# Kernel optimization log

Measured on AMD Instinct MI355X. Metric: run time of the kernel, lower is better.

Reference implementation:

```python
import math
import jax, jax.numpy as jnp
import numpy as np

B, H, HKV, L, S, D = 1, 32, 8, 2048, 2048, 128
N_REP = H // HKV          # 4
SCALE = 1.0 / math.sqrt(D)


def setup_inputs() -> dict:
    key = jax.random.key(0)
    k1, k2, k3, k4 = jax.random.split(key, 4)
    query = jax.random.normal(k1, (B, H, L, D), dtype=jnp.float32)
    k_ = jax.random.normal(k2, (B, HKV, S, D), dtype=jnp.float32)
    v_ = jax.random.normal(k3, (B, HKV, S, D), dtype=jnp.float32)
    attn_mask = jax.random.normal(k4, (B, 1, L, S), dtype=jnp.float32)
    return {"query": query, "key": k_, "value": v_, "attn_mask": attn_mask}


def reference(query, key, value, attn_mask):
    # repeat_kv: Q -> [B, HKV, n_rep, L, D]; K/V stay [B, HKV, S, D]
    # (the torch code reshapes K/V to [B, HKV, 1, S, D]; broadcasting via
    # einsum is equivalent), mask unsqueezed at dim 1 -> [B, 1, 1, L, S].
    q = query.reshape(B, HKV, N_REP, L, D)
    scores = jnp.einsum("bkrld,bksd->bkrls", q, key)          # [B,HKV,n_rep,L,S]
    scores = scores + attn_mask[:, None]                        # broadcast add
    # softmax_fp8(x, dim=-1, invAttnHead=1/sqrt(D)) scales input by invAttnHead
    w = jax.nn.softmax(scores * SCALE, axis=-1)
    # dropout_p = 0.0 -> identity
    out = jnp.einsum("bkrls,bksd->bkrld", w, value)             # [B,HKV,n_rep,L,D]
    return out
```

## Files before the change

kernel.cpp:

```cpp
#include <hip/hip_runtime.h>

#define NH   32
#define NKV  8
#define LQ   2048
#define SK   2048
#define DH   128
#define BM   128
#define BN   64
#define NT   (SK / BN)
#define VSTRIDE 72

typedef __attribute__((ext_vector_type(8)))  short bf8;
typedef __attribute__((ext_vector_type(16))) float f16v;
typedef __attribute__((ext_vector_type(4)))  unsigned int u32x4;

#define CL2E 0.12754308753f

#if __has_builtin(__builtin_amdgcn_exp2f)
#define EXP2F(x) __builtin_amdgcn_exp2f(x)
#else
#define EXP2F(x) exp2f(x)
#endif

__device__ __forceinline__ unsigned short f2bf(float f) {
    unsigned int u = __builtin_bit_cast(unsigned int, f);
    u = (u + 0x7FFFu + ((u >> 16) & 1u)) >> 16;
    return (unsigned short)u;
}

__device__ __forceinline__ unsigned int cvtpk_bf16(float lo, float hi) {
    unsigned int r;
    asm("v_cvt_pk_bf16_f32 %0, %1, %2" : "=v"(r) : "v"(lo), "v"(hi));
    return r;
}

__device__ __forceinline__ float bflo(unsigned int u) {
    return __builtin_bit_cast(float, u << 16);
}
__device__ __forceinline__ float bfhi(unsigned int u) {
    return __builtin_bit_cast(float, u & 0xFFFF0000u);
}

#define GLOAD_LDS16(g, l)                                                      \
    __builtin_amdgcn_global_load_lds(                                          \
        (const __attribute__((address_space(1))) void*)(g),                    \
        (__attribute__((address_space(3))) void*)(l), 16, 0, 0)

__global__ __launch_bounds__(256) void convert_k_kernel(
    const float* __restrict__ K, unsigned short* __restrict__ Kb)
{
    unsigned int cid = blockIdx.x * 256 + threadIdx.x;
    unsigned int p   = cid & 15;
    unsigned int row = cid >> 4;
    unsigned int s   = row & (SK - 1);
    unsigned int c   = p ^ (s & 15);
    const float* src = K + (size_t)row * DH + c * 8;
    float4 a = *(const float4*)(src);
    float4 b = *(const float4*)(src + 4);
    bf8 o;
    o[0] = (short)f2bf(a.x); o[1] = (short)f2bf(a.y);
    o[2] = (short)f2bf(a.z); o[3] = (short)f2bf(a.w);
    o[4] = (short)f2bf(b.x); o[5] = (short)f2bf(b.y);
    o[6] = (short)f2bf(b.z); o[7] = (short)f2bf(b.w);
    *(bf8*)(Kb + (size_t)row * DH + p * 8) = o;
}

__global__ __launch_bounds__(256) void transpose_v_kernel(
    const float* __restrict__ V, unsigned short* __restrict__ VTb)
{
    __shared__ __align__(16) unsigned short Vl[DH * VSTRIDE];
    const int tid = threadIdx.x;
    const int kv  = blockIdx.x >> 5;
    const int t   = blockIdx.x & 31;
    const int s0  = t * 64;
    const float* Vh = V + (size_t)kv * SK * DH;

    #pragma unroll
    for (int i = 0; i < 8; ++i) {
        int idx = tid * 4 + i * 1024;
        int s = idx >> 7, d = idx & 127;
        const float4 v4 = *(const float4*)(Vh + (size_t)(s0 + s) * DH + d);
        Vl[(d + 0) * VSTRIDE + s] = f2bf(v4.x);
        Vl[(d + 1) * VSTRIDE + s] = f2bf(v4.y);
        Vl[(d + 2) * VSTRIDE + s] = f2bf(v4.z);
        Vl[(d + 3) * VSTRIDE + s] = f2bf(v4.w);
    }
    __syncthreads();
    unsigned short* out = VTb + (size_t)(kv * 32 + t) * (DH * 64);
    #pragma unroll
    for (int i = 0; i < 4; ++i) {
        int c = tid + i * 256;
        int d = c >> 3, p = c & 7;
        int sc = (p ^ (d & 7)) * 8;
        *(bf8*)(out + d * 64 + p * 8) = *(const bf8*)(Vl + d * VSTRIDE + sc);
    }
}

__global__ __launch_bounds__(256) void convert_m_kernel(
    const float* __restrict__ M, unsigned short* __restrict__ Mb)
{
    unsigned int cid = blockIdx.x * 256 + threadIdx.x;
    unsigned int row = cid >> 8;
    unsigned int l   = (cid & 255) * 8;
    unsigned int T   = l & ~63u;
    unsigned int loc = l & 63;
    unsigned int mt = loc >> 5, w = loc & 31;
    unsigned int hh = w >> 4, g0 = (w >> 2) & 3;
    const float* src = M + (size_t)row * SK + T + mt * 32 + hh * 4;
    float4 a = *(const float4*)(src + g0 * 8);
    float4 b = *(const float4*)(src + (g0 + 1) * 8);
    bf8 o;
    o[0] = (short)f2bf(a.x * CL2E); o[1] = (short)f2bf(a.y * CL2E);
    o[2] = (short)f2bf(a.z * CL2E); o[3] = (short)f2bf(a.w * CL2E);
    o[4] = (short)f2bf(b.x * CL2E); o[5] = (short)f2bf(b.y * CL2E);
    o[6] = (short)f2bf(b.z * CL2E); o[7] = (short)f2bf(b.w * CL2E);
    *(bf8*)(Mb + (size_t)row * SK + l) = o;
}

__global__ __launch_bounds__(256, 2) void fattn_kernel(
    const float* __restrict__ Q, const unsigned short* __restrict__ Kb,
    const unsigned short* __restrict__ VTb, const unsigned short* __restrict__ Mb,
    float* __restrict__ O)
{
    __shared__ __align__(1024) unsigned char smem[65536];
    unsigned char* KB = smem;
    unsigned char* VB = smem + 32768;

    const int tid  = threadIdx.x;
    const int wave = tid >> 6;
    const int lane = tid & 63;
    const int l32  = lane & 31;
    const int hh   = lane >> 5;

    const int bx = ((int)blockIdx.x & 7) * 64 + ((int)blockIdx.x >> 3);
    const int h  = bx >> 4;
    const int lt = bx & 15;
    const int q0 = lt * BM;
    const int kv = h >> 2;

    const float* Qh = Q + (size_t)h * LQ * DH;
    const unsigned char* Kg = (const unsigned char*)(Kb  + (size_t)kv * SK * DH);
    const unsigned char* Vg = (const unsigned char*)(VTb + (size_t)kv * SK * DH);

    const int qrow = q0 + wave * 32 + l32;
    const unsigned short* Mq = Mb + (size_t)qrow * SK + hh * 16;

    bf8 bQ[8];
    {
        const float* qp = Qh + (size_t)qrow * DH + hh * 8;
        #pragma unroll
        for (int ks = 0; ks < 8; ++ks) {
            float4 a = *(const float4*)(qp + ks * 16);
            float4 b = *(const float4*)(qp + ks * 16 + 4);
            bf8 o;
            o[0] = (short)f2bf(a.x); o[1] = (short)f2bf(a.y);
            o[2] = (short)f2bf(a.z); o[3] = (short)f2bf(a.w);
            o[4] = (short)f2bf(b.x); o[5] = (short)f2bf(b.y);
            o[6] = (short)f2bf(b.z); o[7] = (short)f2bf(b.w);
            bQ[ks] = o;
        }
    }

    const int krow0 = l32 * 256 + ((hh * 16) ^ ((l32 & 15) << 4));
    const int vrowz = l32 * 128 + ((hh * 16) ^ ((l32 & 7) << 4));

    const int stoff = wave * 4096 + lane * 16;

    f16v accO[4];
    #pragma unroll
    for (int dt = 0; dt < 4; ++dt)
        #pragma unroll
        for (int r = 0; r < 16; ++r) accO[dt][r] = 0.f;
    float lpart = 0.f;

    #pragma unroll
    for (int c = 0; c < 4; ++c) GLOAD_LDS16(Kg + stoff + c * 1024, KB + stoff + c * 1024);
    #pragma unroll
    for (int c = 0; c < 4; ++c) GLOAD_LDS16(Vg + stoff + c * 1024, VB + stoff + c * 1024);

    for (int t = 0; t < NT; ++t) {
        const int cur = t & 1;

        const unsigned short* mp = Mq + t * 64;
        u32x4 mA0 = *(const u32x4*)(mp);
        u32x4 mB0 = *(const u32x4*)(mp + 8);
        u32x4 mA1 = *(const u32x4*)(mp + 32);
        u32x4 mB1 = *(const u32x4*)(mp + 40);
        __builtin_amdgcn_sched_barrier(0);

        {
            const int tn = (t + 1) & (NT - 1);
            const unsigned char* ksrc = Kg + (size_t)tn * 16384 + stoff;
            const unsigned char* vsrc = Vg + (size_t)tn * 16384 + stoff;
            unsigned char* kdst = KB + (cur ^ 1) * 16384 + stoff;
            unsigned char* vdst = VB + (cur ^ 1) * 16384 + stoff;
            #pragma unroll
            for (int c = 0; c < 4; ++c) GLOAD_LDS16(ksrc + c * 1024, kdst + c * 1024);
            #pragma unroll
            for (int c = 0; c < 4; ++c) GLOAD_LDS16(vsrc + c * 1024, vdst + c * 1024);
        }
        __builtin_amdgcn_sched_barrier(0);
        asm volatile("s_waitcnt vmcnt(12)" ::: "memory");
        __builtin_amdgcn_s_barrier();
        asm volatile("" ::: "memory");

        const unsigned char* kb = KB + cur * 16384;
        const unsigned char* vb = VB + cur * 16384;

        unsigned int pk0[8], pk1[8];
        #pragma unroll
        for (int mt = 0; mt < 2; ++mt) {
            f16v s;
            #pragma unroll
            for (int r = 0; r < 16; ++r) s[r] = 0.f;
            __builtin_amdgcn_s_setprio(1);
            #pragma unroll
            for (int ks = 0; ks < 8; ++ks) {
                bf8 aK = *(const bf8*)(kb + mt * 8192 + (krow0 ^ (ks << 5)));
                s = __builtin_amdgcn_mfma_f32_32x32x16_bf16(aK, bQ[ks], s, 0, 0, 0);
            }
            __builtin_amdgcn_s_setprio(0);
            const u32x4 mA = mt ? mA1 : mA0;
            const u32x4 mB = mt ? mB1 : mB0;
            unsigned int* pk = mt ? pk1 : pk0;
            #pragma unroll
            for (int g = 0; g < 4; ++g) {
                unsigned int u0 = (g < 2) ? mA[g * 2 + 0] : mB[(g - 2) * 2 + 0];
                unsigned int u1 = (g < 2) ? mA[g * 2 + 1] : mB[(g - 2) * 2 + 1];
                float e0 = EXP2F(fmaf(s[g*4+0], CL2E, bflo(u0)));
                float e1 = EXP2F(fmaf(s[g*4+1], CL2E, bfhi(u0)));
                float e2 = EXP2F(fmaf(s[g*4+2], CL2E, bflo(u1)));
                float e3 = EXP2F(fmaf(s[g*4+3], CL2E, bfhi(u1)));
                lpart += (e0 + e1) + (e2 + e3);
                pk[g*2+0] = cvtpk_bf16(e0, e1);
                pk[g*2+1] = cvtpk_bf16(e2, e3);
            }
        }

        bf8 bP[4];
        #pragma unroll
        for (int ks = 0; ks < 4; ++ks) {
            unsigned int* pk = (ks >> 1) ? pk1 : pk0;
            const int kk = ks & 1;
            unsigned int a0 = pk[kk*4+0], b0 = pk[kk*4+2];
            unsigned int a1 = pk[kk*4+1], b1 = pk[kk*4+3];
            asm volatile("v_permlane32_swap_b32 %0, %1" : "+v"(a0), "+v"(b0));
            asm volatile("v_permlane32_swap_b32 %0, %1" : "+v"(a1), "+v"(b1));
            u32x4 w; w[0] = a0; w[1] = a1; w[2] = b0; w[3] = b1;
            bP[ks] = __builtin_bit_cast(bf8, w);
        }

        __builtin_amdgcn_s_setprio(1);
        #pragma unroll
        for (int dt = 0; dt < 4; ++dt) {
            #pragma unroll
            for (int ks = 0; ks < 4; ++ks) {
                bf8 aV = *(const bf8*)(vb + dt * 4096 + (vrowz ^ (ks << 5)));
                accO[dt] = __builtin_amdgcn_mfma_f32_32x32x16_bf16(aV, bP[ks], accO[dt], 0, 0, 0);
            }
        }
        __builtin_amdgcn_s_setprio(0);
        asm volatile("" ::: "memory");
        __builtin_amdgcn_s_barrier();
        asm volatile("" ::: "memory");
    }

    asm volatile("s_waitcnt vmcnt(0)" ::: "memory");
    float l = lpart + __shfl_xor(lpart, 32);
    float inv = 1.0f / l;
    float* Op = O + (size_t)h * LQ * DH + (size_t)qrow * DH;
    #pragma unroll
    for (int dt = 0; dt < 4; ++dt) {
        #pragma unroll
        for (int g = 0; g < 4; ++g) {
            int d = dt * 32 + g * 8 + hh * 4;
            float4 o;
            o.x = accO[dt][g * 4 + 0] * inv;
            o.y = accO[dt][g * 4 + 1] * inv;
            o.z = accO[dt][g * 4 + 2] * inv;
            o.w = accO[dt][g * 4 + 3] * inv;
            *(float4*)(Op + d) = o;
        }
    }
}

extern "C" void kernel_launch(void* const* d_in, const int* in_sizes, int n_in,
                              void* d_out, int out_size, void* d_ws, size_t ws_size,
                              hipStream_t stream) {
    const float* Q = (const float*)d_in[0];
    const float* K = (const float*)d_in[1];
    const float* V = (const float*)d_in[2];
    const float* M = (const float*)d_in[3];
    float* O = (float*)d_out;

    unsigned short* Kb  = (unsigned short*)d_ws;
    unsigned short* VTb = Kb + (size_t)NKV * SK * DH;
    unsigned short* Mb  = VTb + (size_t)NKV * DH * SK;

    convert_k_kernel<<<dim3((NKV * SK * 16) / 256), 256, 0, stream>>>(K, Kb);
    transpose_v_kernel<<<dim3(NKV * (SK / 64)), 256, 0, stream>>>(V, VTb);
    convert_m_kernel<<<dim3((LQ * (SK / 8)) / 256), 256, 0, stream>>>(M, Mb);

    dim3 grid(NH * (LQ / BM));
    fattn_kernel<<<grid, 256, 0, stream>>>(Q, Kb, VTb, Mb, O);
}
```

Measured before the change: 185.1 us.

## Split KV tile across wave pairs, halve query tile, merge prep kernels

Halves the query tile per block to 64 rows and splits each 64-key tile between pairs of waves, each handling 32 keys. Partial outputs and row sums are reduced through shared memory at the end. V is now staged through registers into a single LDS buffer, which cuts LDS to 48KB so three blocks fit per CU. The three preprocessing kernels are also merged into one launch. The aim is higher occupancy and fewer launches, at the cost of an extra cross-wave reduction and more grid blocks reloading K/V.

Result: slower. 228.0 us (+23.2%).

```diff
diff --git a/kernel.cpp b/kernel.cpp
--- a/kernel.cpp
+++ b/kernel.cpp
@@ -5,7 +5,7 @@
 #define LQ   2048
 #define SK   2048
 #define DH   128
-#define BM   128
+#define BM   64
 #define BN   64
 #define NT   (SK / BN)
 #define VSTRIDE 72
@@ -46,83 +46,81 @@
         (const __attribute__((address_space(1))) void*)(g),                    \
         (__attribute__((address_space(3))) void*)(l), 16, 0, 0)
 
-__global__ __launch_bounds__(256) void convert_k_kernel(
-    const float* __restrict__ K, unsigned short* __restrict__ Kb)
-{
-    unsigned int cid = blockIdx.x * 256 + threadIdx.x;
-    unsigned int p   = cid & 15;
-    unsigned int row = cid >> 4;
-    unsigned int s   = row & (SK - 1);
-    unsigned int c   = p ^ (s & 15);
-    const float* src = K + (size_t)row * DH + c * 8;
-    float4 a = *(const float4*)(src);
-    float4 b = *(const float4*)(src + 4);
-    bf8 o;
-    o[0] = (short)f2bf(a.x); o[1] = (short)f2bf(a.y);
-    o[2] = (short)f2bf(a.z); o[3] = (short)f2bf(a.w);
-    o[4] = (short)f2bf(b.x); o[5] = (short)f2bf(b.y);
-    o[6] = (short)f2bf(b.z); o[7] = (short)f2bf(b.w);
-    *(bf8*)(Kb + (size_t)row * DH + p * 8) = o;
-}
-
-__global__ __launch_bounds__(256) void transpose_v_kernel(
-    const float* __restrict__ V, unsigned short* __restrict__ VTb)
+__global__ __launch_bounds__(256) void prep_kernel(
+    const float* __restrict__ K, unsigned short* __restrict__ Kb,
+    const float* __restrict__ V, unsigned short* __restrict__ VTb,
+    const float* __restrict__ M, unsigned short* __restrict__ Mb)
 {
     __shared__ __align__(16) unsigned short Vl[DH * VSTRIDE];
     const int tid = threadIdx.x;
-    const int kv  = blockIdx.x >> 5;
-    const int t   = blockIdx.x & 31;
-    const int s0  = t * 64;
-    const float* Vh = V + (size_t)kv * SK * DH;
-
-    #pragma unroll
-    for (int i = 0; i < 8; ++i) {
-        int idx = tid * 4 + i * 1024;
-        int s = idx >> 7, d = idx & 127;
-        const float4 v4 = *(const float4*)(Vh + (size_t)(s0 + s) * DH + d);
-        Vl[(d + 0) * VSTRIDE + s] = f2bf(v4.x);
-        Vl[(d + 1) * VSTRIDE + s] = f2bf(v4.y);
-        Vl[(d + 2) * VSTRIDE + s] = f2bf(v4.z);
-        Vl[(d + 3) * VSTRIDE + s] = f2bf(v4.w);
-    }
-    __syncthreads();
-    unsigned short* out = VTb + (size_t)(kv * 32 + t) * (DH * 64);
-    #pragma unroll
-    for (int i = 0; i < 4; ++i) {
-        int c = tid + i * 256;
-        int d = c >> 3, p = c & 7;
-        int sc = (p ^ (d & 7)) * 8;
-        *(bf8*)(out + d * 64 + p * 8) = *(const bf8*)(Vl + d * VSTRIDE + sc);
-    }
-}
-
-__global__ __launch_bounds__(256) void convert_m_kernel(
-    const float* __restrict__ M, unsigned short* __restrict__ Mb)
-{
-    unsigned int cid = blockIdx.x * 256 + threadIdx.x;
-    unsigned int row = cid >> 8;
-    unsigned int l   = (cid & 255) * 8;
-    unsigned int T   = l & ~63u;
-    unsigned int loc = l & 63;
-    unsigned int mt = loc >> 5, w = loc & 31;
-    unsigned int hh = w >> 4, g0 = (w >> 2) & 3;
-    const float* src = M + (size_t)row * SK + T + mt * 32 + hh * 4;
-    float4 a = *(const float4*)(src + g0 * 8);
-    float4 b = *(const float4*)(src + (g0 + 1) * 8);
-    bf8 o;
-    o[0] = (short)f2bf(a.x * CL2E); o[1] = (short)f2bf(a.y * CL2E);
-    o[2] = (short)f2bf(a.z * CL2E); o[3] = (short)f2bf(a.w * CL2E);
-    o[4] = (short)f2bf(b.x * CL2E); o[5] = (short)f2bf(b.y * CL2E);
-    o[6] = (short)f2bf(b.z * CL2E); o[7] = (short)f2bf(b.w * CL2E);
-    *(bf8*)(Mb + (size_t)row * SK + l) = o;
-}
-
-__global__ __launch_bounds__(256, 2) void fattn_kernel(
+    const int bid = blockIdx.x;
+
+    if (bid < 1024) {
+        unsigned int cid = bid * 256 + tid;
+        unsigned int p   = cid & 15;
+        unsigned int row = cid >> 4;
+        unsigned int s   = row & (SK - 1);
+        unsigned int c   = p ^ (s & 15);
+        const float* src = K + (size_t)row * DH + c * 8;
+        float4 a = *(const float4*)(src);
+        float4 b = *(const float4*)(src + 4);
+        bf8 o;
+        o[0] = (short)f2bf(a.x); o[1] = (short)f2bf(a.y);
+        o[2] = (short)f2bf(a.z); o[3] = (short)f2bf(a.w);
+        o[4] = (short)f2bf(b.x); o[5] = (short)f2bf(b.y);
+        o[6] = (short)f2bf(b.z); o[7] = (short)f2bf(b.w);
+        *(bf8*)(Kb + (size_t)row * DH + p * 8) = o;
+    } else if (bid < 1280) {
+        const int vb = bid - 1024;
+        const int kv = vb >> 5;
+        const int t  = vb & 31;
+        const int s0 = t * 64;
+        const float* Vh = V + (size_t)kv * SK * DH;
+        #pragma unroll
+        for (int i = 0; i < 8; ++i) {
+            int idx = tid * 4 + i * 1024;
+            int s = idx >> 7, d = idx & 127;
+            const float4 v4 = *(const float4*)(Vh + (size_t)(s0 + s) * DH + d);
+            Vl[(d + 0) * VSTRIDE + s] = f2bf(v4.x);
+            Vl[(d + 1) * VSTRIDE + s] = f2bf(v4.y);
+            Vl[(d + 2) * VSTRIDE + s] = f2bf(v4.z);
+            Vl[(d + 3) * VSTRIDE + s] = f2bf(v4.w);
+        }
+        __syncthreads();
+        unsigned short* out = VTb + (size_t)(kv * 32 + t) * (DH * 64);
+        #pragma unroll
+        for (int i = 0; i < 4; ++i) {
+            int c = tid + i * 256;
+            int d = c >> 3, p = c & 7;
+            int sc = (p ^ (d & 7)) * 8;
+            *(bf8*)(out + d * 64 + p * 8) = *(const bf8*)(Vl + d * VSTRIDE + sc);
+        }
+    } else {
+        unsigned int cid = (bid - 1280) * 256 + tid;
+        unsigned int row = cid >> 8;
+        unsigned int l   = (cid & 255) * 8;
+        unsigned int T   = l & ~63u;
+        unsigned int loc = l & 63;
+        unsigned int mt = loc >> 5, w = loc & 31;
+        unsigned int hh = w >> 4, g0 = (w >> 2) & 3;
+        const float* src = M + (size_t)row * SK + T + mt * 32 + hh * 4;
+        float4 a = *(const float4*)(src + g0 * 8);
+        float4 b = *(const float4*)(src + (g0 + 1) * 8);
+        bf8 o;
+        o[0] = (short)f2bf(a.x * CL2E); o[1] = (short)f2bf(a.y * CL2E);
+        o[2] = (short)f2bf(a.z * CL2E); o[3] = (short)f2bf(a.w * CL2E);
+        o[4] = (short)f2bf(b.x * CL2E); o[5] = (short)f2bf(b.y * CL2E);
+        o[6] = (short)f2bf(b.z * CL2E); o[7] = (short)f2bf(b.w * CL2E);
+        *(bf8*)(Mb + (size_t)row * SK + l) = o;
+    }
+}
+
+__global__ __launch_bounds__(256, 3) void fattn_kernel(
     const float* __restrict__ Q, const unsigned short* __restrict__ Kb,
     const unsigned short* __restrict__ VTb, const unsigned short* __restrict__ Mb,
     float* __restrict__ O)
 {
-    __shared__ __align__(1024) unsigned char smem[65536];
+    __shared__ __align__(1024) unsigned char smem[49152];
     unsigned char* KB = smem;
     unsigned char* VB = smem + 32768;
 
@@ -131,10 +129,12 @@
     const int lane = tid & 63;
     const int l32  = lane & 31;
     const int hh   = lane >> 5;
-
-    const int bx = ((int)blockIdx.x & 7) * 64 + ((int)blockIdx.x >> 3);
-    const int h  = bx >> 4;
-    const int lt = bx & 15;
+    const int qg   = wave >> 1;
+    const int sg   = wave & 1;
+
+    const int bx = ((int)blockIdx.x & 7) * 128 + ((int)blockIdx.x >> 3);
+    const int h  = bx >> 5;
+    const int lt = bx & 31;
     const int q0 = lt * BM;
     const int kv = h >> 2;
 
@@ -142,8 +142,8 @@
     const unsigned char* Kg = (const unsigned char*)(Kb  + (size_t)kv * SK * DH);
     const unsigned char* Vg = (const unsigned char*)(VTb + (size_t)kv * SK * DH);
 
-    const int qrow = q0 + wave * 32 + l32;
-    const unsigned short* Mq = Mb + (size_t)qrow * SK + hh * 16;
+    const int qrow = q0 + qg * 32 + l32;
+    const unsigned short* Mq = Mb + (size_t)qrow * SK + sg * 32 + hh * 16;
 
     bf8 bQ[8];
     {
@@ -161,10 +161,8 @@
         }
     }
 
-    const int krow0 = l32 * 256 + ((hh * 16) ^ ((l32 & 15) << 4));
-    const int vrowz = l32 * 128 + ((hh * 16) ^ ((l32 & 7) << 4));
-
-    const int stoff = wave * 4096 + lane * 16;
+    const int krow0 = (sg * 32 + l32) * 256 + ((hh * 16) ^ ((l32 & 15) << 4));
+    const int vrow0 = l32 * 128 + ((sg * 64 + hh * 16) ^ ((l32 & 7) << 4));
 
     f16v accO[4];
     #pragma unroll
@@ -173,77 +171,78 @@
         for (int r = 0; r < 16; ++r) accO[dt][r] = 0.f;
     float lpart = 0.f;
 
-    #pragma unroll
-    for (int c = 0; c < 4; ++c) GLOAD_LDS16(Kg + stoff + c * 1024, KB + stoff + c * 1024);
-    #pragma unroll
-    for (int c = 0; c < 4; ++c) GLOAD_LDS16(Vg + stoff + c * 1024, VB + stoff + c * 1024);
+    {
+        const int so = wave * 1024 + lane * 16;
+        #pragma unroll
+        for (int c = 0; c < 4; ++c) GLOAD_LDS16(Kg + so + c * 4096, KB + so + c * 4096);
+        #pragma unroll
+        for (int c = 0; c < 4; ++c) GLOAD_LDS16(Vg + so + c * 4096, VB + so + c * 4096);
+    }
+
+    u32x4 vr0, vr1, vr2, vr3;
 
     for (int t = 0; t < NT; ++t) {
         const int cur = t & 1;
 
         const unsigned short* mp = Mq + t * 64;
-        u32x4 mA0 = *(const u32x4*)(mp);
-        u32x4 mB0 = *(const u32x4*)(mp + 8);
-        u32x4 mA1 = *(const u32x4*)(mp + 32);
-        u32x4 mB1 = *(const u32x4*)(mp + 40);
+        u32x4 mA = *(const u32x4*)(mp);
+        u32x4 mB = *(const u32x4*)(mp + 8);
         __builtin_amdgcn_sched_barrier(0);
 
+        const int tn = (t + 1) & (NT - 1);
         {
-            const int tn = (t + 1) & (NT - 1);
-            const unsigned char* ksrc = Kg + (size_t)tn * 16384 + stoff;
-            const unsigned char* vsrc = Vg + (size_t)tn * 16384 + stoff;
-            unsigned char* kdst = KB + (cur ^ 1) * 16384 + stoff;
-            unsigned char* vdst = VB + (cur ^ 1) * 16384 + stoff;
-            #pragma unroll
-            for (int c = 0; c < 4; ++c) GLOAD_LDS16(ksrc + c * 1024, kdst + c * 1024);
-            #pragma unroll
-            for (int c = 0; c < 4; ++c) GLOAD_LDS16(vsrc + c * 1024, vdst + c * 1024);
+            const unsigned char* vsrc = Vg + (size_t)tn * 16384 + tid * 64;
+            vr0 = *(const u32x4*)(vsrc);
+            vr1 = *(const u32x4*)(vsrc + 16);
+            vr2 = *(const u32x4*)(vsrc + 32);
+            vr3 = *(const u32x4*)(vsrc + 48);
         }
         __builtin_amdgcn_sched_barrier(0);
-        asm volatile("s_waitcnt vmcnt(12)" ::: "memory");
+
+        {
+            const unsigned char* ksrc = Kg + (size_t)tn * 16384;
+            unsigned char* kdst = KB + (cur ^ 1) * 16384;
+            const int so = wave * 1024 + lane * 16;
+            #pragma unroll
+            for (int c = 0; c < 4; ++c) GLOAD_LDS16(ksrc + so + c * 4096, kdst + so + c * 4096);
+        }
+        __builtin_amdgcn_sched_barrier(0);
+        asm volatile("s_waitcnt vmcnt(10) lgkmcnt(0)" ::: "memory");
         __builtin_amdgcn_s_barrier();
         asm volatile("" ::: "memory");
 
         const unsigned char* kb = KB + cur * 16384;
-        const unsigned char* vb = VB + cur * 16384;
-
-        unsigned int pk0[8], pk1[8];
-        #pragma unroll
-        for (int mt = 0; mt < 2; ++mt) {
-            f16v s;
-            #pragma unroll
-            for (int r = 0; r < 16; ++r) s[r] = 0.f;
-            __builtin_amdgcn_s_setprio(1);
-            #pragma unroll
-            for (int ks = 0; ks < 8; ++ks) {
-                bf8 aK = *(const bf8*)(kb + mt * 8192 + (krow0 ^ (ks << 5)));
-                s = __builtin_amdgcn_mfma_f32_32x32x16_bf16(aK, bQ[ks], s, 0, 0, 0);
-            }
-            __builtin_amdgcn_s_setprio(0);
-            const u32x4 mA = mt ? mA1 : mA0;
-            const u32x4 mB = mt ? mB1 : mB0;
-            unsigned int* pk = mt ? pk1 : pk0;
-            #pragma unroll
-            for (int g = 0; g < 4; ++g) {
-                unsigned int u0 = (g < 2) ? mA[g * 2 + 0] : mB[(g - 2) * 2 + 0];
-                unsigned int u1 = (g < 2) ? mA[g * 2 + 1] : mB[(g - 2) * 2 + 1];
-                float e0 = EXP2F(fmaf(s[g*4+0], CL2E, bflo(u0)));
-                float e1 = EXP2F(fmaf(s[g*4+1], CL2E, bfhi(u0)));
-                float e2 = EXP2F(fmaf(s[g*4+2], CL2E, bflo(u1)));
-                float e3 = EXP2F(fmaf(s[g*4+3], CL2E, bfhi(u1)));
-                lpart += (e0 + e1) + (e2 + e3);
-                pk[g*2+0] = cvtpk_bf16(e0, e1);
-                pk[g*2+1] = cvtpk_bf16(e2, e3);
-            }
-        }
-
-        bf8 bP[4];
-        #pragma unroll
-        for (int ks = 0; ks < 4; ++ks) {
-            unsigned int* pk = (ks >> 1) ? pk1 : pk0;
-            const int kk = ks & 1;
-            unsigned int a0 = pk[kk*4+0], b0 = pk[kk*4+2];
-            unsigned int a1 = pk[kk*4+1], b1 = pk[kk*4+3];
+
+        f16v s;
+        #pragma unroll
+        for (int r = 0; r < 16; ++r) s[r] = 0.f;
+        __builtin_amdgcn_s_setprio(1);
+        #pragma unroll
+        for (int ks = 0; ks < 8; ++ks) {
+            bf8 aK = *(const bf8*)(kb + (krow0 ^ (ks << 5)));
+            s = __builtin_amdgcn_mfma_f32_32x32x16_bf16(aK, bQ[ks], s, 0, 0, 0);
+        }
+        __builtin_amdgcn_s_setprio(0);
+
+        unsigned int pk[8];
+        #pragma unroll
+        for (int g = 0; g < 4; ++g) {
+            unsigned int u0 = (g < 2) ? mA[g * 2 + 0] : mB[(g - 2) * 2 + 0];
+            unsigned int u1 = (g < 2) ? mA[g * 2 + 1] : mB[(g - 2) * 2 + 1];
+            float e0 = EXP2F(fmaf(s[g*4+0], CL2E, bflo(u0)));
+            float e1 = EXP2F(fmaf(s[g*4+1], CL2E, bfhi(u0)));
+            float e2 = EXP2F(fmaf(s[g*4+2], CL2E, bflo(u1)));
+            float e3 = EXP2F(fmaf(s[g*4+3], CL2E, bfhi(u1)));
+            lpart += (e0 + e1) + (e2 + e3);
+            pk[g*2+0] = cvtpk_bf16(e0, e1);
+            pk[g*2+1] = cvtpk_bf16(e2, e3);
+        }
+
+        bf8 bP[2];
+        #pragma unroll
+        for (int ks = 0; ks < 2; ++ks) {
+            unsigned int a0 = pk[ks*4+0], b0 = pk[ks*4+2];
+            unsigned int a1 = pk[ks*4+1], b1 = pk[ks*4+3];
             asm volatile("v_permlane32_swap_b32 %0, %1" : "+v"(a0), "+v"(b0));
             asm volatile("v_permlane32_swap_b32 %0, %1" : "+v"(a1), "+v"(b1));
             u32x4 w; w[0] = a0; w[1] = a1; w[2] = b0; w[3] = b1;
@@ -254,8 +253,8 @@
         #pragma unroll
         for (int dt = 0; dt < 4; ++dt) {
             #pragma unroll
-            for (int ks = 0; ks < 4; ++ks) {
-                bf8 aV = *(const bf8*)(vb + dt * 4096 + (vrowz ^ (ks << 5)));
+            for (int ks = 0; ks < 2; ++ks) {
+                bf8 aV = *(const bf8*)(VB + dt * 4096 + (vrow0 ^ (ks << 5)));
                 accO[dt] = __builtin_amdgcn_mfma_f32_32x32x16_bf16(aV, bP[ks], accO[dt], 0, 0, 0);
             }
         }
@@ -263,23 +262,73 @@
         asm volatile("" ::: "memory");
         __builtin_amdgcn_s_barrier();
         asm volatile("" ::: "memory");
-    }
-
-    asm volatile("s_waitcnt vmcnt(0)" ::: "memory");
-    float l = lpart + __shfl_xor(lpart, 32);
-    float inv = 1.0f / l;
+
+        if (t + 1 < NT) {
+            unsigned char* vdst = VB + tid * 64;
+            *(u32x4*)(vdst)      = vr0;
+            *(u32x4*)(vdst + 16) = vr1;
+            *(u32x4*)(vdst + 32) = vr2;
+            *(u32x4*)(vdst + 48) = vr3;
+        }
+    }
+
+    asm volatile("s_waitcnt vmcnt(0) lgkmcnt(0)" ::: "memory");
+    __builtin_amdgcn_s_barrier();
+    asm volatile("" ::: "memory");
+    float* xs  = (float*)smem;
+    float* lsc = (float*)(smem + 40960);
+    const int pw = qg * 2 + (sg ^ 1);
+    lsc[wave * 64 + lane] = lpart;
+    if (sg == 1) {
+        #pragma unroll
+        for (int dt = 0; dt < 2; ++dt)
+            #pragma unroll
+            for (int r = 0; r < 16; ++r)
+                xs[((qg * 2 + dt) * 16 + r) * 64 + lane] = accO[dt][r];
+    }
+    asm volatile("s_waitcnt lgkmcnt(0)" ::: "memory");
+    __builtin_amdgcn_s_barrier();
+    asm volatile("" ::: "memory");
+    float l = lpart + lsc[pw * 64 + lane];
+    l += __shfl_xor(l, 32);
+    const float inv = 1.0f / l;
     float* Op = O + (size_t)h * LQ * DH + (size_t)qrow * DH;
-    #pragma unroll
-    for (int dt = 0; dt < 4; ++dt) {
-        #pragma unroll
-        for (int g = 0; g < 4; ++g) {
-            int d = dt * 32 + g * 8 + hh * 4;
-            float4 o;
-            o.x = accO[dt][g * 4 + 0] * inv;
-            o.y = accO[dt][g * 4 + 1] * inv;
-            o.z = accO[dt][g * 4 + 2] * inv;
-            o.w = accO[dt][g * 4 + 3] * inv;
-            *(float4*)(Op + d) = o;
+    if (sg == 0) {
+        #pragma unroll
+        for (int dt = 0; dt < 2; ++dt) {
+            #pragma unroll
+            for (int g = 0; g < 4; ++g) {
+                const int xb = ((qg * 2 + dt) * 16 + g * 4) * 64 + lane;
+                float4 o;
+                o.x = (accO[dt][g*4+0] + xs[xb +   0]) * inv;
+                o.y = (accO[dt][g*4+1] + xs[xb +  64]) * inv;
+                o.z = (accO[dt][g*4+2] + xs[xb + 128]) * inv;
+                o.w = (accO[dt][g*4+3] + xs[xb + 192]) * inv;
+                *(float4*)(Op + dt * 32 + g * 8 + hh * 4) = o;
+            }
+        }
+        #pragma unroll
+        for (int dt = 0; dt < 2; ++dt)
+            #pragma unroll
+            for (int r = 0; r < 16; ++r)
+                xs[((qg * 2 + dt) * 16 + r) * 64 + lane] = accO[dt + 2][r];
+    }
+    asm volatile("s_waitcnt lgkmcnt(0)" ::: "memory");
+    __builtin_amdgcn_s_barrier();
+    asm volatile("" ::: "memory");
+    if (sg == 1) {
+        #pragma unroll
+        for (int dt = 0; dt < 2; ++dt) {
+            #pragma unroll
+            for (int g = 0; g < 4; ++g) {
+                const int xb = ((qg * 2 + dt) * 16 + g * 4) * 64 + lane;
+                float4 o;
+                o.x = (accO[dt+2][g*4+0] + xs[xb +   0]) * inv;
+                o.y = (accO[dt+2][g*4+1] + xs[xb +  64]) * inv;
+                o.z = (accO[dt+2][g*4+2] + xs[xb + 128]) * inv;
+                o.w = (accO[dt+2][g*4+3] + xs[xb + 192]) * inv;
+                *(float4*)(Op + (dt + 2) * 32 + g * 8 + hh * 4) = o;
+            }
         }
     }
 }
@@ -297,9 +346,7 @@
     unsigned short* VTb = Kb + (size_t)NKV * SK * DH;
     unsigned short* Mb  = VTb + (size_t)NKV * DH * SK;
 
-    convert_k_kernel<<<dim3((NKV * SK * 16) / 256), 256, 0, stream>>>(K, Kb);
-    transpose_v_kernel<<<dim3(NKV * (SK / 64)), 256, 0, stream>>>(V, VTb);
-    convert_m_kernel<<<dim3((LQ * (SK / 8)) / 256), 256, 0, stream>>>(M, Mb);
+    prep_kernel<<<dim3(3328), 256, 0, stream>>>(K, Kb, V, VTb, M, Mb);
 
     dim3 grid(NH * (LQ / BM));
     fattn_kernel<<<grid, 256, 0, stream>>>(Q, Kb, VTb, Mb, O);
```

## Merge prep kernels into one launch and restructure LDS loads ahead of MFMAs

Applied to the files above, without the earlier changes.

The three preprocessing kernels (K convert, V transpose, mask convert) become a single kernel that dispatches on block index, removing two launches and the gaps between them. In the attention loop, K fragments are batch-loaded from LDS before each MFMA chain, both QK tiles are computed before the softmax exps, and part of the V fragments are prefetched ahead of the exp work so LDS reads overlap ALU work. The row-sum accumulator is split into two partials. Holding more fragments live raises register pressure, which could hurt occupancy at the two-blocks-per-CU launch bound, and every prep block now allocates the V-transpose shared buffer.

Result: no change. 181.7 us (-1.8%).

```diff
diff --git a/kernel.cpp b/kernel.cpp
--- a/kernel.cpp
+++ b/kernel.cpp
@@ -46,75 +46,73 @@
         (const __attribute__((address_space(1))) void*)(g),                    \
         (__attribute__((address_space(3))) void*)(l), 16, 0, 0)
 
-__global__ __launch_bounds__(256) void convert_k_kernel(
-    const float* __restrict__ K, unsigned short* __restrict__ Kb)
-{
-    unsigned int cid = blockIdx.x * 256 + threadIdx.x;
-    unsigned int p   = cid & 15;
-    unsigned int row = cid >> 4;
-    unsigned int s   = row & (SK - 1);
-    unsigned int c   = p ^ (s & 15);
-    const float* src = K + (size_t)row * DH + c * 8;
-    float4 a = *(const float4*)(src);
-    float4 b = *(const float4*)(src + 4);
-    bf8 o;
-    o[0] = (short)f2bf(a.x); o[1] = (short)f2bf(a.y);
-    o[2] = (short)f2bf(a.z); o[3] = (short)f2bf(a.w);
-    o[4] = (short)f2bf(b.x); o[5] = (short)f2bf(b.y);
-    o[6] = (short)f2bf(b.z); o[7] = (short)f2bf(b.w);
-    *(bf8*)(Kb + (size_t)row * DH + p * 8) = o;
-}
-
-__global__ __launch_bounds__(256) void transpose_v_kernel(
-    const float* __restrict__ V, unsigned short* __restrict__ VTb)
+__global__ __launch_bounds__(256) void prep_kernel(
+    const float* __restrict__ K, unsigned short* __restrict__ Kb,
+    const float* __restrict__ V, unsigned short* __restrict__ VTb,
+    const float* __restrict__ M, unsigned short* __restrict__ Mb)
 {
     __shared__ __align__(16) unsigned short Vl[DH * VSTRIDE];
     const int tid = threadIdx.x;
-    const int kv  = blockIdx.x >> 5;
-    const int t   = blockIdx.x & 31;
-    const int s0  = t * 64;
-    const float* Vh = V + (size_t)kv * SK * DH;
-
-    #pragma unroll
-    for (int i = 0; i < 8; ++i) {
-        int idx = tid * 4 + i * 1024;
-        int s = idx >> 7, d = idx & 127;
-        const float4 v4 = *(const float4*)(Vh + (size_t)(s0 + s) * DH + d);
-        Vl[(d + 0) * VSTRIDE + s] = f2bf(v4.x);
-        Vl[(d + 1) * VSTRIDE + s] = f2bf(v4.y);
-        Vl[(d + 2) * VSTRIDE + s] = f2bf(v4.z);
-        Vl[(d + 3) * VSTRIDE + s] = f2bf(v4.w);
+    const int bid = blockIdx.x;
+
+    if (bid < 1024) {
+        unsigned int cid = bid * 256 + tid;
+        unsigned int p   = cid & 15;
+        unsigned int row = cid >> 4;
+        unsigned int s   = row & (SK - 1);
+        unsigned int c   = p ^ (s & 15);
+        const float* src = K + (size_t)row * DH + c * 8;
+        float4 a = *(const float4*)(src);
+        float4 b = *(const float4*)(src + 4);
+        bf8 o;
+        o[0] = (short)f2bf(a.x); o[1] = (short)f2bf(a.y);
+        o[2] = (short)f2bf(a.z); o[3] = (short)f2bf(a.w);
+        o[4] = (short)f2bf(b.x); o[5] = (short)f2bf(b.y);
+        o[6] = (short)f2bf(b.z); o[7] = (short)f2bf(b.w);
+        *(bf8*)(Kb + (size_t)row * DH + p * 8) = o;
+    } else if (bid < 1280) {
+        const int vb = bid - 1024;
+        const int kv = vb >> 5;
+        const int t  = vb & 31;
+        const int s0 = t * 64;
+        const float* Vh = V + (size_t)kv * SK * DH;
+        #pragma unroll
+        for (int i = 0; i < 8; ++i) {
+            int idx = tid * 4 + i * 1024;
+            int s = idx >> 7, d = idx & 127;
+            const float4 v4 = *(const float4*)(Vh + (size_t)(s0 + s) * DH + d);
+            Vl[(d + 0) * VSTRIDE + s] = f2bf(v4.x);
+            Vl[(d + 1) * VSTRIDE + s] = f2bf(v4.y);
+            Vl[(d + 2) * VSTRIDE + s] = f2bf(v4.z);
+            Vl[(d + 3) * VSTRIDE + s] = f2bf(v4.w);
+        }
+        __syncthreads();
+        unsigned short* out = VTb + (size_t)(kv * 32 + t) * (DH * 64);
+        #pragma unroll
+        for (int i = 0; i < 4; ++i) {
+            int c = tid + i * 256;
+            int d = c >> 3, p = c & 7;
+            int sc = (p ^ (d & 7)) * 8;
+            *(bf8*)(out + d * 64 + p * 8) = *(const bf8*)(Vl + d * VSTRIDE + sc);
+        }
+    } else {
+        unsigned int cid = (bid - 1280) * 256 + tid;
+        unsigned int row = cid >> 8;
+        unsigned int l   = (cid & 255) * 8;
+        unsigned int T   = l & ~63u;
+        unsigned int loc = l & 63;
+        unsigned int mt = loc >> 5, w = loc & 31;
+        unsigned int hh = w >> 4, g0 = (w >> 2) & 3;
+        const float* src = M + (size_t)row * SK + T + mt * 32 + hh * 4;
+        float4 a = *(const float4*)(src + g0 * 8);
+        float4 b = *(const float4*)(src + (g0 + 1) * 8);
+        bf8 o;
+        o[0] = (short)f2bf(a.x * CL2E); o[1] = (short)f2bf(a.y * CL2E);
+        o[2] = (short)f2bf(a.z * CL2E); o[3] = (short)f2bf(a.w * CL2E);
+        o[4] = (short)f2bf(b.x * CL2E); o[5] = (short)f2bf(b.y * CL2E);
+        o[6] = (short)f2bf(b.z * CL2E); o[7] = (short)f2bf(b.w * CL2E);
+        *(bf8*)(Mb + (size_t)row * SK + l) = o;
     }
-    __syncthreads();
-    unsigned short* out = VTb + (size_t)(kv * 32 + t) * (DH * 64);
-    #pragma unroll
-    for (int i = 0; i < 4; ++i) {
-        int c = tid + i * 256;
-        int d = c >> 3, p = c & 7;
-        int sc = (p ^ (d & 7)) * 8;
-        *(bf8*)(out + d * 64 + p * 8) = *(const bf8*)(Vl + d * VSTRIDE + sc);
-    }
-}
-
-__global__ __launch_bounds__(256) void convert_m_kernel(
-    const float* __restrict__ M, unsigned short* __restrict__ Mb)
-{
-    unsigned int cid = blockIdx.x * 256 + threadIdx.x;
-    unsigned int row = cid >> 8;
-    unsigned int l   = (cid & 255) * 8;
-    unsigned int T   = l & ~63u;
-    unsigned int loc = l & 63;
-    unsigned int mt = loc >> 5, w = loc & 31;
-    unsigned int hh = w >> 4, g0 = (w >> 2) & 3;
-    const float* src = M + (size_t)row * SK + T + mt * 32 + hh * 4;
-    float4 a = *(const float4*)(src + g0 * 8);
-    float4 b = *(const float4*)(src + (g0 + 1) * 8);
-    bf8 o;
-    o[0] = (short)f2bf(a.x * CL2E); o[1] = (short)f2bf(a.y * CL2E);
-    o[2] = (short)f2bf(a.z * CL2E); o[3] = (short)f2bf(a.w * CL2E);
-    o[4] = (short)f2bf(b.x * CL2E); o[5] = (short)f2bf(b.y * CL2E);
-    o[6] = (short)f2bf(b.z * CL2E); o[7] = (short)f2bf(b.w * CL2E);
-    *(bf8*)(Mb + (size_t)row * SK + l) = o;
 }
 
 __global__ __launch_bounds__(256, 2) void fattn_kernel(
@@ -171,7 +169,7 @@
     for (int dt = 0; dt < 4; ++dt)
         #pragma unroll
         for (int r = 0; r < 16; ++r) accO[dt][r] = 0.f;
-    float lpart = 0.f;
+    float lpA = 0.f, lpB = 0.f;
 
     #pragma unroll
     for (int c = 0; c < 4; ++c) GLOAD_LDS16(Kg + stoff + c * 1024, KB + stoff + c * 1024);
@@ -207,34 +205,60 @@
         const unsigned char* kb = KB + cur * 16384;
         const unsigned char* vb = VB + cur * 16384;
 
+        f16v s0, s1;
+        #pragma unroll
+        for (int r = 0; r < 16; ++r) { s0[r] = 0.f; s1[r] = 0.f; }
+        {
+            bf8 aK[8];
+            #pragma unroll
+            for (int ks = 0; ks < 8; ++ks)
+                aK[ks] = *(const bf8*)(kb + (krow0 ^ (ks << 5)));
+            __builtin_amdgcn_s_setprio(1);
+            #pragma unroll
+            for (int ks = 0; ks < 8; ++ks)
+                s0 = __builtin_amdgcn_mfma_f32_32x32x16_bf16(aK[ks], bQ[ks], s0, 0, 0, 0);
+            __builtin_amdgcn_s_setprio(0);
+            #pragma unroll
+            for (int ks = 0; ks < 8; ++ks)
+                aK[ks] = *(const bf8*)(kb + 8192 + (krow0 ^ (ks << 5)));
+            __builtin_amdgcn_s_setprio(1);
+            #pragma unroll
+            for (int ks = 0; ks < 8; ++ks)
+                s1 = __builtin_amdgcn_mfma_f32_32x32x16_bf16(aK[ks], bQ[ks], s1, 0, 0, 0);
+            __builtin_amdgcn_s_setprio(0);
+        }
+
+        bf8 aV0[4];
+        #pragma unroll
+        for (int dt = 0; dt < 2; ++dt)
+            #pragma unroll
+            for (int ks = 0; ks < 2; ++ks)
+                aV0[dt*2+ks] = *(const bf8*)(vb + dt * 4096 + (vrowz ^ (ks << 5)));
+
         unsigned int pk0[8], pk1[8];
         #pragma unroll
-        for (int mt = 0; mt < 2; ++mt) {
-            f16v s;
-            #pragma unroll
-            for (int r = 0; r < 16; ++r) s[r] = 0.f;
-            __builtin_amdgcn_s_setprio(1);
-            #pragma unroll
-            for (int ks = 0; ks < 8; ++ks) {
-                bf8 aK = *(const bf8*)(kb + mt * 8192 + (krow0 ^ (ks << 5)));
-                s = __builtin_amdgcn_mfma_f32_32x32x16_bf16(aK, bQ[ks], s, 0, 0, 0);
-            }
-            __builtin_amdgcn_s_setprio(0);
-            const u32x4 mA = mt ? mA1 : mA0;
-            const u32x4 mB = mt ? mB1 : mB0;
-            unsigned int* pk = mt ? pk1 : pk0;
-            #pragma unroll
-            for (int g = 0; g < 4; ++g) {
-                unsigned int u0 = (g < 2) ? mA[g * 2 + 0] : mB[(g - 2) * 2 + 0];
-                unsigned int u1 = (g < 2) ? mA[g * 2 + 1] : mB[(g - 2) * 2 + 1];
-                float e0 = EXP2F(fmaf(s[g*4+0], CL2E, bflo(u0)));
-                float e1 = EXP2F(fmaf(s[g*4+1], CL2E, bfhi(u0)));
-                float e2 = EXP2F(fmaf(s[g*4+2], CL2E, bflo(u1)));
-                float e3 = EXP2F(fmaf(s[g*4+3], CL2E, bfhi(u1)));
-                lpart += (e0 + e1) + (e2 + e3);
-                pk[g*2+0] = cvtpk_bf16(e0, e1);
-                pk[g*2+1] = cvtpk_bf16(e2, e3);
-            }
+        for (int g = 0; g < 4; ++g) {
+            unsigned int u0 = (g < 2) ? mA0[g * 2 + 0] : mB0[(g - 2) * 2 + 0];
+            unsigned int u1 = (g < 2) ? mA0[g * 2 + 1] : mB0[(g - 2) * 2 + 1];
+            float e0 = EXP2F(fmaf(s0[g*4+0], CL2E, bflo(u0)));
+            float e1 = EXP2F(fmaf(s0[g*4+1], CL2E, bfhi(u0)));
+            float e2 = EXP2F(fmaf(s0[g*4+2], CL2E, bflo(u1)));
+            float e3 = EXP2F(fmaf(s0[g*4+3], CL2E, bfhi(u1)));
+            lpA += (e0 + e1) + (e2 + e3);
+            pk0[g*2+0] = cvtpk_bf16(e0, e1);
+            pk0[g*2+1] = cvtpk_bf16(e2, e3);
+        }
+        #pragma unroll
+        for (int g = 0; g < 4; ++g) {
+            unsigned int u0 = (g < 2) ? mA1[g * 2 + 0] : mB1[(g - 2) * 2 + 0];
+            unsigned int u1 = (g < 2) ? mA1[g * 2 + 1] : mB1[(g - 2) * 2 + 1];
+            float e0 = EXP2F(fmaf(s1[g*4+0], CL2E, bflo(u0)));
+            float e1 = EXP2F(fmaf(s1[g*4+1], CL2E, bfhi(u0)));
+            float e2 = EXP2F(fmaf(s1[g*4+2], CL2E, bflo(u1)));
+            float e3 = EXP2F(fmaf(s1[g*4+3], CL2E, bfhi(u1)));
+            lpB += (e0 + e1) + (e2 + e3);
+            pk1[g*2+0] = cvtpk_bf16(e0, e1);
+            pk1[g*2+1] = cvtpk_bf16(e2, e3);
         }
 
         bf8 bP[4];
@@ -250,22 +274,47 @@
             bP[ks] = __builtin_bit_cast(bf8, w);
         }
 
+        bf8 aV1[4];
+        #pragma unroll
+        for (int dt = 0; dt < 2; ++dt)
+            #pragma unroll
+            for (int ks = 0; ks < 2; ++ks)
+                aV1[dt*2+ks] = *(const bf8*)(vb + (dt + 2) * 4096 + (vrowz ^ (ks << 5)));
+
         __builtin_amdgcn_s_setprio(1);
         #pragma unroll
-        for (int dt = 0; dt < 4; ++dt) {
-            #pragma unroll
-            for (int ks = 0; ks < 4; ++ks) {
-                bf8 aV = *(const bf8*)(vb + dt * 4096 + (vrowz ^ (ks << 5)));
-                accO[dt] = __builtin_amdgcn_mfma_f32_32x32x16_bf16(aV, bP[ks], accO[dt], 0, 0, 0);
+        for (int dt = 0; dt < 2; ++dt) {
+            accO[dt] = __builtin_amdgcn_mfma_f32_32x32x16_bf16(aV0[dt*2+0], bP[0], accO[dt], 0, 0, 0);
+            accO[dt] = __builtin_amdgcn_mfma_f32_32x32x16_bf16(aV0[dt*2+1], bP[1], accO[dt], 0, 0, 0);
+        }
+        #pragma unroll
+        for (int dt = 0; dt < 2; ++dt) {
+            accO[dt+2] = __builtin_amdgcn_mfma_f32_32x32x16_bf16(aV1[dt*2+0], bP[0], accO[dt+2], 0, 0, 0);
+            accO[dt+2] = __builtin_amdgcn_mfma_f32_32x32x16_bf16(aV1[dt*2+1], bP[1], accO[dt+2], 0, 0, 0);
+        }
+        __builtin_amdgcn_s_setprio(0);
+        {
+            bf8 aV2[8];
+            #pragma unroll
+            for (int dt = 0; dt < 4; ++dt)
+                #pragma unroll
+                for (int ks = 2; ks < 4; ++ks)
+                    aV2[dt*2+(ks-2)] = *(const bf8*)(vb + dt * 4096 + (vrowz ^ (ks << 5)));
+            __builtin_amdgcn_s_setprio(1);
+            #pragma unroll
+            for (int dt = 0; dt < 4; ++dt) {
+                accO[dt] = __builtin_amdgcn_mfma_f32_32x32x16_bf16(aV2[dt*2+0], bP[2], accO[dt], 0, 0, 0);
+                accO[dt] = __builtin_amdgcn_mfma_f32_32x32x16_bf16(aV2[dt*2+1], bP[3], accO[dt], 0, 0, 0);
             }
-        }
-        __builtin_amdgcn_s_setprio(0);
+            __builtin_amdgcn_s_setprio(0);
+        }
         asm volatile("" ::: "memory");
         __builtin_amdgcn_s_barrier();
         asm volatile("" ::: "memory");
     }
 
     asm volatile("s_waitcnt vmcnt(0)" ::: "memory");
+    float lpart = lpA + lpB;
     float l = lpart + __shfl_xor(lpart, 32);
     float inv = 1.0f / l;
     float* Op = O + (size_t)h * LQ * DH + (size_t)qrow * DH;
@@ -297,9 +346,7 @@
     unsigned short* VTb = Kb + (size_t)NKV * SK * DH;
     unsigned short* Mb  = VTb + (size_t)NKV * DH * SK;
 
-    convert_k_kernel<<<dim3((NKV * SK * 16) / 256), 256, 0, stream>>>(K, Kb);
-    transpose_v_kernel<<<dim3(NKV * (SK / 64)), 256, 0, stream>>>(V, VTb);
-    convert_m_kernel<<<dim3((LQ * (SK / 8)) / 256), 256, 0, stream>>>(M, Mb);
+    prep_kernel<<<dim3(3328), 256, 0, stream>>>(K, Kb, V, VTb, M, Mb);
 
     dim3 grid(NH * (LQ / BM));
     fattn_kernel<<<grid, 256, 0, stream>>>(Q, Kb, VTb, Mb, O);
```
